# Kernel optimization log

Hardware: AMD Instinct MI355X
Metric: run time of the kernel (lower is better)

Reference implementation:

```python
import jax, jax.numpy as jnp
import numpy as np

TEMPERATURE = 0.1
K = 5  # hard-coded k=5 in ANDCriterion.forward
EPS = 1e-12  # F.normalize eps


def setup_inputs() -> dict:
    key = jax.random.key(0)
    z = jax.random.normal(key, (8192, 1024), dtype=jnp.float32)
    return {"z": z}


def _normalize(z):
    nrm = jnp.sqrt(jnp.sum(z * z, axis=1, keepdims=True))
    return z / jnp.maximum(nrm, EPS)


def reference(z):
    n = z.shape[0]
    zn = _normalize(z)                      # [N, d], L2-normalized rows
    sim = zn @ zn.T                         # [N, N] cosine similarity
    # kNN neighbors (exclude self, which is always the top-1 hit)
    _, idx = jax.lax.top_k(sim, K + 1)      # [N, K+1]
    neigh = idx[:, 1:]                      # [N, K]
    # AND loss: softmax over non-self entries at temperature T;
    # loss_i = -log sum_{j in N(i)} p_ij
    logits = sim / TEMPERATURE
    logits = jnp.where(jnp.eye(n, dtype=bool), -jnp.inf, logits)
    logp = jax.nn.log_softmax(logits, axis=1)           # [N, N]
    neigh_logp = jnp.take_along_axis(logp, neigh, axis=1)  # [N, K]
    loss = -jnp.mean(jax.nn.logsumexp(neigh_logp, axis=1))
    return loss
```

## Files before the change

### kernel.cpp

```cpp
#include <hip/hip_runtime.h>
#include <stdint.h>

#define N_ROWS 8192
#define D_DIM  1024
#define NEG_BIG -1e30f
#define NCHUNK 32
#define CHUNK_J 256
#define NTILE 8
#define BUFSZ 17408

typedef __attribute__((ext_vector_type(16))) float f32x16;
typedef __attribute__((ext_vector_type(8)))  int   i32x8;
typedef __attribute__((ext_vector_type(4)))  int   i32x4;
typedef __attribute__((ext_vector_type(2)))  long  long2_t;

#define EXPC 14.4269504089f
#define EXPRAW(dst, v) { float _a = fmaf((v), EXPC, -EXPC);                 \
    asm("v_exp_f32 %0, %1" : "=v"(dst) : "v"(_a)); }

#define INS5(b0,b1,b2,b3,b4,v) {                        \
    float _n4 = __builtin_amdgcn_fmed3f(b3, (v), b4);   \
    float _n3 = __builtin_amdgcn_fmed3f(b2, (v), b3);   \
    float _n2 = __builtin_amdgcn_fmed3f(b1, (v), b2);   \
    float _n1 = __builtin_amdgcn_fmed3f(b0, (v), b1);   \
    b0 = fmaxf(b0, (v)); b1 = _n1; b2 = _n2; b3 = _n3; b4 = _n4; }

static __device__ inline uint32_t enc4(float x, float inv) {
    float q = fabsf(x) * inv;
    uint32_t n = q < 0.25f ? 0u : (q < 0.75f ? 1u : (q < 1.25f ? 2u : (q < 1.75f ? 3u :
                 (q < 2.5f  ? 4u : (q < 3.5f  ? 5u : (q < 5.0f  ? 6u : 7u))))));
    return n | (x < 0.f ? 8u : 0u);
}

__global__ __launch_bounds__(256) void norm_kernel(const float* __restrict__ z,
                                                   uint8_t* __restrict__ zn4,
                                                   uint8_t* __restrict__ sbq) {
    int wave = threadIdx.x >> 6;
    int lane = threadIdx.x & 63;
    int row  = blockIdx.x * 4 + wave;
    const float* zr = z + (size_t)row * D_DIM;
    float4 c[4];
    float ss = 0.f;
#pragma unroll
    for (int i = 0; i < 4; ++i) {
        c[i] = *(const float4*)(zr + i * 256 + lane * 4);
        ss += c[i].x*c[i].x + c[i].y*c[i].y + c[i].z*c[i].z + c[i].w*c[i].w;
    }
#pragma unroll
    for (int m = 1; m < 64; m <<= 1) ss += __shfl_xor(ss, m);
    float scale = 1.0f / fmaxf(sqrtf(ss), 1e-12f);
    const int J = row >> 5, r31 = row & 31;
    uint8_t* db = zn4 + (size_t)J * 16384;
    uint8_t* sb = sbq + (size_t)J * 1024;
#pragma unroll
    for (int i = 0; i < 4; ++i) {
        float x0 = c[i].x*scale, x1 = c[i].y*scale, x2 = c[i].z*scale, x3 = c[i].w*scale;
        float am = fmaxf(fmaxf(fabsf(x0), fabsf(x1)), fmaxf(fabsf(x2), fabsf(x3)));
        am = fmaxf(am, __shfl_xor(am, 1));
        am = fmaxf(am, __shfl_xor(am, 2));
        am = fmaxf(am, __shfl_xor(am, 4));
        uint32_t ub = __float_as_uint(am);
        int sbyte = (int)(ub >> 23) - 2 + (((ub & 0x7fffffu) > 0x400000u) ? 1 : 0);
        float inv = __uint_as_float((uint32_t)(254 - sbyte) << 23);
        uint32_t pk = enc4(x0, inv) | (enc4(x1, inv) << 4)
                    | (enc4(x2, inv) << 8) | (enc4(x3, inv) << 12);
        int m  = i * 4 + (lane >> 4);
        int l2 = r31 + 32 * ((lane >> 3) & 1);
        *(uint16_t*)(db + m * 1024 + l2 * 16 + 2 * (lane & 7)) = (uint16_t)pk;
        if ((lane & 7) == 0) {
            int j = lane >> 3;
            sb[(size_t)(r31 + 32 * (j & 1)) * 16 + i * 4 + (j >> 1)] = (uint8_t)sbyte;
        }
    }
}

__global__ __launch_bounds__(256, 3) void sim_kernel(const uint8_t* __restrict__ zn4,
                                                     const uint8_t* __restrict__ sbq,
                                                     float* __restrict__ pstats) {
    __shared__ __align__(16) char lds[2 * BUFSZ];
    const int tid  = threadIdx.x;
    const int w    = tid >> 6;
    const int l    = tid & 63;
    const int r32  = l & 31;
    const int h    = l >> 5;
    const int ib   = blockIdx.x >> 5;
    const int ch   = blockIdx.x & 31;
    const int i0w  = ib * 128 + w * 32;
    const int j0c  = ch * CHUNK_J;
    const int i_lane = i0w + r32;
    const int Ii   = ib * 4 + w;
    const int diag_jt = ((Ii >> 3) == ch) ? (Ii & 7) : -1;
    const char* ldsr = lds + l * 16;

#define GLL(SRC, DST) __builtin_amdgcn_global_load_lds(                         \
        (const __attribute__((address_space(1))) uint32_t*)(SRC),               \
        (__attribute__((address_space(3))) uint32_t*)(DST), 16, 0, 0)

#define STAGE(JTN, BUF) {                                                       \
        const uint8_t* sD_ = zn4 + (size_t)(ch * NTILE + (JTN)) * 16384;        \
        _Pragma("unroll")                                                       \
        for (int mm = 0; mm < 4; ++mm) {                                        \
            int m_ = w * 4 + mm;                                                \
            GLL(sD_ + m_ * 1024 + l * 16, (BUF) + m_ * 1024);                   \
        }                                                                       \
        if (w == 0)                                                             \
            GLL(sbq + (size_t)(ch * NTILE + (JTN)) * 1024 + l * 16,             \
                (BUF) + 16384);                                                 \
    }

    STAGE(0, lds);

    i32x8 bres8[8];
    {
        const uint8_t* rp = zn4 + (size_t)Ii * 16384 + l * 16;
#pragma unroll
        for (int g = 0; g < 8; ++g) {
            *(long2_t*)&bres8[g]       = *(const long2_t*)(rp + (2 * g) * 1024);
            *((long2_t*)&bres8[g] + 1) = *(const long2_t*)(rp + (2 * g + 1) * 1024);
        }
    }
    uint32_t sb_[4];
    {
        const uint32_t* sp = (const uint32_t*)(sbq + (size_t)Ii * 1024 + l * 16);
        sb_[0] = sp[0]; sb_[1] = sp[1]; sb_[2] = sp[2]; sb_[3] = sp[3];
    }

    float s0r = 0.f, s1r = 0.f;
    float b0 = NEG_BIG, b1 = NEG_BIG, b2 = NEG_BIG, b3 = NEG_BIG, b4 = NEG_BIG;
    i32x8 areg0 = {0,0,0,0,0,0,0,0}, areg1 = {0,0,0,0,0,0,0,0};
    i32x8 btmp  = {0,0,0,0,0,0,0,0};

    __syncthreads();

#define MFMA_E(M) {                                                             \
        asm volatile("" : "+v"(bres8[(M) >> 1]));                               \
        *(long2_t*)&areg0 = *(const long2_t*)(ldst_ + (M) * 1024);              \
        acc0 = __builtin_amdgcn_mfma_scale_f32_32x32x64_f8f6f4(                 \
            areg0, bres8[(M) >> 1], acc0, 4, 4,                                 \
            (M) & 3, sa_[(M) >> 2], (M) & 3, sb_[(M) >> 2]); }
#define MFMA_O(M) {                                                             \
        *(long2_t*)&btmp  = *((const long2_t*)&bres8[(M) >> 1] + 1);            \
        *(long2_t*)&areg1 = *(const long2_t*)(ldst_ + (M) * 1024);              \
        acc1 = __builtin_amdgcn_mfma_scale_f32_32x32x64_f8f6f4(                 \
            areg1, btmp, acc1, 4, 4,                                            \
            (M) & 3, sa_[(M) >> 2], (M) & 3, sb_[(M) >> 2]); }

#define TILE_BODY(JT, CUR) {                                                    \
        if ((JT) + 1 < NTILE) STAGE((JT) + 1, lds + ((CUR) ^ BUFSZ));           \
        const char* ldst_ = ldsr + (CUR);                                       \
        uint32_t sa_[4];                                                        \
        {                                                                       \
            i32x4 sv = *(const i32x4*)(lds + (CUR) + 16384 + l * 16);           \
            sa_[0] = sv[0]; sa_[1] = sv[1]; sa_[2] = sv[2]; sa_[3] = sv[3];     \
        }                                                                       \
        f32x16 acc0, acc1;                                                      \
        _Pragma("unroll")                                                       \
        for (int r = 0; r < 16; ++r) { acc0[r] = 0.f; acc1[r] = 0.f; }          \
        __builtin_amdgcn_s_setprio(1);                                          \
        MFMA_E(0)  MFMA_O(1)  MFMA_E(2)  MFMA_O(3)                              \
        MFMA_E(4)  MFMA_O(5)  MFMA_E(6)  MFMA_O(7)                              \
        MFMA_E(8)  MFMA_O(9)  MFMA_E(10) MFMA_O(11)                             \
        MFMA_E(12) MFMA_O(13) MFMA_E(14) MFMA_O(15)                             \
        __builtin_amdgcn_s_setprio(0);                                          \
        if ((JT) != diag_jt) {                                                  \
            _Pragma("unroll")                                                   \
            for (int r = 0; r < 16; ++r) {                                      \
                float v = acc0[r] + acc1[r];                                    \
                INS5(b0, b1, b2, b3, b4, v);                                    \
                float e_; EXPRAW(e_, v);                                        \
                if (r & 1) s1r += e_; else s0r += e_;                           \
            }                                                                   \
        } else {                                                                \
            const int dd2 = i_lane - (j0c + (JT) * 32) - 4 * h;                 \
            _Pragma("unroll")                                                   \
            for (int r = 0; r < 16; ++r) {                                      \
                const int jm = (r & 3) + 8 * (r >> 2);                          \
                float v = acc0[r] + acc1[r];                                    \
                if (dd2 == jm) v = NEG_BIG;                                     \
                INS5(b0, b1, b2, b3, b4, v);                                    \
                float e_; EXPRAW(e_, v);                                        \
                if (r & 1) s1r += e_; else s0r += e_;                           \
            }                                                                   \
        }                                                                       \
        __syncthreads();                                                        \
    }

    for (int jt = 0; jt < NTILE; jt += 2) {
        TILE_BODY(jt, 0);
        TILE_BODY(jt + 1, BUFSZ);
    }
#undef TILE_BODY
#undef MFMA_E
#undef MFMA_O
#undef STAGE
#undef GLL

    float s_run = s0r + s1r;
    s_run += __shfl_xor(s_run, 32);
    {
        float o0 = __shfl_xor(b0, 32), o1 = __shfl_xor(b1, 32), o2 = __shfl_xor(b2, 32),
              o3 = __shfl_xor(b3, 32), o4 = __shfl_xor(b4, 32);
        INS5(b0, b1, b2, b3, b4, o0); INS5(b0, b1, b2, b3, b4, o1);
        INS5(b0, b1, b2, b3, b4, o2); INS5(b0, b1, b2, b3, b4, o3);
        INS5(b0, b1, b2, b3, b4, o4);
    }
    if (h == 0) {
        float* p = pstats + ((size_t)ch * N_ROWS + i_lane) * 8;
        p[0] = s_run; p[1] = b0; p[2] = b1; p[3] = b2; p[4] = b3; p[5] = b4;
        p[6] = 0.f; p[7] = 0.f;
    }
}

__global__ __launch_bounds__(128) void reduce1(const float* __restrict__ pstats,
                                               float* __restrict__ partial) {
    int row = blockIdx.x * 128 + threadIdx.x;
    float S = 0.f;
    float b0 = NEG_BIG, b1 = NEG_BIG, b2 = NEG_BIG, b3 = NEG_BIG, b4 = NEG_BIG;
#pragma unroll
    for (int c = 0; c < NCHUNK; ++c) {
        const float* p = pstats + ((size_t)c * N_ROWS + row) * 8;
        S += p[0];
        float v0 = p[1], v1 = p[2], v2 = p[3], v3 = p[4], v4 = p[5];
        INS5(b0, b1, b2, b3, b4, v0); INS5(b0, b1, b2, b3, b4, v1);
        INS5(b0, b1, b2, b3, b4, v2); INS5(b0, b1, b2, b3, b4, v3);
        INS5(b0, b1, b2, b3, b4, v4);
    }
    float e0, e1, e2, e3, e4;
    EXPRAW(e0, b0); EXPRAW(e1, b1); EXPRAW(e2, b2); EXPRAW(e3, b3); EXPRAW(e4, b4);
    float S5 = e0 + e1 + e2 + e3 + e4;
    float loss = __logf(S) - __logf(S5);
#pragma unroll
    for (int m = 1; m < 64; m <<= 1) loss += __shfl_xor(loss, m);
    __shared__ float rr[2];
    if ((threadIdx.x & 63) == 0) rr[threadIdx.x >> 6] = loss;
    __syncthreads();
    if (threadIdx.x == 0) partial[blockIdx.x] = rr[0] + rr[1];
}

__global__ void reduce2(const float* __restrict__ partial, float* __restrict__ out) {
    float v = partial[threadIdx.x];
#pragma unroll
    for (int m = 1; m < 64; m <<= 1) v += __shfl_xor(v, m);
    if (threadIdx.x == 0) out[0] = v * (1.0f / N_ROWS);
}

extern "C" void kernel_launch(void* const* d_in, const int* in_sizes, int n_in,
                              void* d_out, int out_size, void* d_ws, size_t ws_size,
                              hipStream_t stream) {
    const float* z = (const float*)d_in[0];
    float* out = (float*)d_out;
    uint8_t* zn4   = (uint8_t*)d_ws;
    uint8_t* sbq   = (uint8_t*)d_ws + (size_t)4 * 1024 * 1024;
    float* pstats  = (float*)((char*)d_ws + (size_t)4608 * 1024);
    float* partial = (float*)((char*)d_ws + (size_t)13 * 1024 * 1024);

    norm_kernel<<<N_ROWS / 4, 256, 0, stream>>>(z, zn4, sbq);
    sim_kernel<<<64 * NCHUNK, 256, 0, stream>>>(zn4, sbq, pstats);
    reduce1<<<N_ROWS / 128, 128, 0, stream>>>(pstats, partial);
    reduce2<<<1, 64, 0, stream>>>(partial, out);
}
```

Baseline: 69.86 us.

## Fuse final reduction into reduce1 via atomic counter; raise sim occupancy bound

Removes the separate reduce2 launch: each reduce1 block publishes its partial sum with a release store and bumps an atomic counter, and the last block to arrive sums all 64 partials and writes the mean. The counter is reset inside norm_kernel, so it is zero before reduce1 runs. Separately, sim_kernel's launch bounds go from 3 to 4 blocks per SIMD/CU, which pressures the compiler to use fewer registers. That allows more concurrent waves but risks register spills.

Result: slower. 79.69 us (+14.1%).

```diff
diff --git a/kernel.cpp b/kernel.cpp
--- a/kernel.cpp
+++ b/kernel.cpp
@@ -34,7 +34,9 @@
 
 __global__ __launch_bounds__(256) void norm_kernel(const float* __restrict__ z,
                                                    uint8_t* __restrict__ zn4,
-                                                   uint8_t* __restrict__ sbq) {
+                                                   uint8_t* __restrict__ sbq,
+                                                   unsigned* __restrict__ counter) {
+    if (blockIdx.x == 0 && threadIdx.x == 0) *counter = 0;
     int wave = threadIdx.x >> 6;
     int lane = threadIdx.x & 63;
     int row  = blockIdx.x * 4 + wave;
@@ -74,7 +76,7 @@
     }
 }
 
-__global__ __launch_bounds__(256, 3) void sim_kernel(const uint8_t* __restrict__ zn4,
+__global__ __launch_bounds__(256, 4) void sim_kernel(const uint8_t* __restrict__ zn4,
                                                      const uint8_t* __restrict__ sbq,
                                                      float* __restrict__ pstats) {
     __shared__ __align__(16) char lds[2 * BUFSZ];
@@ -85,9 +87,8 @@
     const int h    = l >> 5;
     const int ib   = blockIdx.x >> 5;
     const int ch   = blockIdx.x & 31;
-    const int i0w  = ib * 128 + w * 32;
     const int j0c  = ch * CHUNK_J;
-    const int i_lane = i0w + r32;
+    const int i_lane = ib * 128 + w * 32 + r32;
     const int Ii   = ib * 4 + w;
     const int diag_jt = ((Ii >> 3) == ch) ? (Ii & 7) : -1;
     const char* ldsr = lds + l * 16;
@@ -212,7 +213,9 @@
 }
 
 __global__ __launch_bounds__(128) void reduce1(const float* __restrict__ pstats,
-                                               float* __restrict__ partial) {
+                                               float* __restrict__ partial,
+                                               unsigned* __restrict__ counter,
+                                               float* __restrict__ out) {
     int row = blockIdx.x * 128 + threadIdx.x;
     float S = 0.f;
     float b0 = NEG_BIG, b1 = NEG_BIG, b2 = NEG_BIG, b3 = NEG_BIG, b4 = NEG_BIG;
@@ -234,14 +237,20 @@
     __shared__ float rr[2];
     if ((threadIdx.x & 63) == 0) rr[threadIdx.x >> 6] = loss;
     __syncthreads();
-    if (threadIdx.x == 0) partial[blockIdx.x] = rr[0] + rr[1];
-}
-
-__global__ void reduce2(const float* __restrict__ partial, float* __restrict__ out) {
-    float v = partial[threadIdx.x];
-#pragma unroll
-    for (int m = 1; m < 64; m <<= 1) v += __shfl_xor(v, m);
-    if (threadIdx.x == 0) out[0] = v * (1.0f / N_ROWS);
+    if (threadIdx.x == 0) {
+        float mine = rr[0] + rr[1];
+        __hip_atomic_store(&partial[blockIdx.x], mine,
+                           __ATOMIC_RELEASE, __HIP_MEMORY_SCOPE_AGENT);
+        unsigned prev = __hip_atomic_fetch_add(counter, 1u,
+                           __ATOMIC_ACQ_REL, __HIP_MEMORY_SCOPE_AGENT);
+        if (prev == 63u) {
+            float s = 0.f;
+            for (int i = 0; i < 64; ++i)
+                s += __hip_atomic_load(&partial[i],
+                         __ATOMIC_ACQUIRE, __HIP_MEMORY_SCOPE_AGENT);
+            out[0] = s * (1.0f / N_ROWS);
+        }
+    }
 }
 
 extern "C" void kernel_launch(void* const* d_in, const int* in_sizes, int n_in,
@@ -253,9 +262,9 @@
     uint8_t* sbq   = (uint8_t*)d_ws + (size_t)4 * 1024 * 1024;
     float* pstats  = (float*)((char*)d_ws + (size_t)4608 * 1024);
     float* partial = (float*)((char*)d_ws + (size_t)13 * 1024 * 1024);
-
-    norm_kernel<<<N_ROWS / 4, 256, 0, stream>>>(z, zn4, sbq);
+    unsigned* counter = (unsigned*)((char*)d_ws + (size_t)13 * 1024 * 1024 + 256);
+
+    norm_kernel<<<N_ROWS / 4, 256, 0, stream>>>(z, zn4, sbq, counter);
     sim_kernel<<<64 * NCHUNK, 256, 0, stream>>>(zn4, sbq, pstats);
-    reduce1<<<N_ROWS / 128, 128, 0, stream>>>(pstats, partial);
-    reduce2<<<1, 64, 0, stream>>>(partial, out);
-}
+    reduce1<<<N_ROWS / 128, 128, 0, stream>>>(pstats, partial, counter, out);
+}
```

## Widen column chunks, prefetch A operands ahead, skip top-5 insert when unneeded

Applied to the files above, without the earlier changes.

Doubles the column chunk per block from 256 to 512 (16 tiles), which halves the grid and the partial-stat entries, and lowers launch bounds to 2 waves per SIMD. The MFMA loop now keeps four A registers and loads each operand four MFMAs ahead from LDS, so LDS latency overlaps with matrix work. The top-5 insertion is skipped for a tile unless some lane's tile max beats its current fifth-best value, which avoids many med3 ops. The costs are more register pressure and lower occupancy, and the 50 unseen lines (the reduction kernel) must agree with the new NCHUNK.

After: 69.57 us. About the same (-0.4%).

```diff
diff --git a/kernel.cpp b/kernel.cpp
--- a/kernel.cpp
+++ b/kernel.cpp
@@ -4,9 +4,9 @@
 #define N_ROWS 8192
 #define D_DIM  1024
 #define NEG_BIG -1e30f
-#define NCHUNK 32
-#define CHUNK_J 256
-#define NTILE 8
+#define NCHUNK 16
+#define CHUNK_J 512
+#define NTILE 16
 #define BUFSZ 17408
 
 typedef __attribute__((ext_vector_type(16))) float f32x16;
@@ -74,7 +74,7 @@
     }
 }
 
-__global__ __launch_bounds__(256, 3) void sim_kernel(const uint8_t* __restrict__ zn4,
+__global__ __launch_bounds__(256, 2) void sim_kernel(const uint8_t* __restrict__ zn4,
                                                      const uint8_t* __restrict__ sbq,
                                                      float* __restrict__ pstats) {
     __shared__ __align__(16) char lds[2 * BUFSZ];
@@ -83,13 +83,12 @@
     const int l    = tid & 63;
     const int r32  = l & 31;
     const int h    = l >> 5;
-    const int ib   = blockIdx.x >> 5;
-    const int ch   = blockIdx.x & 31;
-    const int i0w  = ib * 128 + w * 32;
+    const int ib   = blockIdx.x >> 4;
+    const int ch   = blockIdx.x & 15;
     const int j0c  = ch * CHUNK_J;
-    const int i_lane = i0w + r32;
+    const int i_lane = ib * 128 + w * 32 + r32;
     const int Ii   = ib * 4 + w;
-    const int diag_jt = ((Ii >> 3) == ch) ? (Ii & 7) : -1;
+    const int diag_jt = ((Ii >> 4) == ch) ? (Ii & 15) : -1;
     const char* ldsr = lds + l * 16;
 
 #define GLL(SRC, DST) __builtin_amdgcn_global_load_lds(                         \
@@ -127,23 +126,24 @@
 
     float s0r = 0.f, s1r = 0.f;
     float b0 = NEG_BIG, b1 = NEG_BIG, b2 = NEG_BIG, b3 = NEG_BIG, b4 = NEG_BIG;
-    i32x8 areg0 = {0,0,0,0,0,0,0,0}, areg1 = {0,0,0,0,0,0,0,0};
-    i32x8 btmp  = {0,0,0,0,0,0,0,0};
+    i32x8 a0 = {0,0,0,0,0,0,0,0}, a1 = {0,0,0,0,0,0,0,0};
+    i32x8 a2 = {0,0,0,0,0,0,0,0}, a3 = {0,0,0,0,0,0,0,0};
+    i32x8 btmp = {0,0,0,0,0,0,0,0};
 
     __syncthreads();
 
-#define MFMA_E(M) {                                                             \
+#define MFMA_EV(M, AR, RF) {                                                    \
         asm volatile("" : "+v"(bres8[(M) >> 1]));                               \
-        *(long2_t*)&areg0 = *(const long2_t*)(ldst_ + (M) * 1024);              \
         acc0 = __builtin_amdgcn_mfma_scale_f32_32x32x64_f8f6f4(                 \
-            areg0, bres8[(M) >> 1], acc0, 4, 4,                                 \
-            (M) & 3, sa_[(M) >> 2], (M) & 3, sb_[(M) >> 2]); }
-#define MFMA_O(M) {                                                             \
-        *(long2_t*)&btmp  = *((const long2_t*)&bres8[(M) >> 1] + 1);            \
-        *(long2_t*)&areg1 = *(const long2_t*)(ldst_ + (M) * 1024);              \
+            AR, bres8[(M) >> 1], acc0, 4, 4,                                    \
+            (M) & 3, sa_[(M) >> 2], (M) & 3, sb_[(M) >> 2]);                    \
+        if ((RF) >= 0) *(long2_t*)&AR = *(const long2_t*)(ldst_ + (RF) * 1024); }
+#define MFMA_OD(M, AR, RF) {                                                    \
+        *(long2_t*)&btmp = *((const long2_t*)&bres8[(M) >> 1] + 1);             \
         acc1 = __builtin_amdgcn_mfma_scale_f32_32x32x64_f8f6f4(                 \
-            areg1, btmp, acc1, 4, 4,                                            \
-            (M) & 3, sa_[(M) >> 2], (M) & 3, sb_[(M) >> 2]); }
+            AR, btmp, acc1, 4, 4,                                               \
+            (M) & 3, sa_[(M) >> 2], (M) & 3, sb_[(M) >> 2]);                    \
+        if ((RF) >= 0) *(long2_t*)&AR = *(const long2_t*)(ldst_ + (RF) * 1024); }
 
 #define TILE_BODY(JT, CUR) {                                                    \
         if ((JT) + 1 < NTILE) STAGE((JT) + 1, lds + ((CUR) ^ BUFSZ));           \
@@ -153,34 +153,46 @@
             i32x4 sv = *(const i32x4*)(lds + (CUR) + 16384 + l * 16);           \
             sa_[0] = sv[0]; sa_[1] = sv[1]; sa_[2] = sv[2]; sa_[3] = sv[3];     \
         }                                                                       \
+                                   \
+        *(long2_t*)&a0 = *(const long2_t*)(ldst_ + 0 * 1024);                   \
+        *(long2_t*)&a1 = *(const long2_t*)(ldst_ + 1 * 1024);                   \
+        *(long2_t*)&a2 = *(const long2_t*)(ldst_ + 2 * 1024);                   \
+        *(long2_t*)&a3 = *(const long2_t*)(ldst_ + 3 * 1024);                   \
         f32x16 acc0, acc1;                                                      \
         _Pragma("unroll")                                                       \
         for (int r = 0; r < 16; ++r) { acc0[r] = 0.f; acc1[r] = 0.f; }          \
         __builtin_amdgcn_s_setprio(1);                                          \
-        MFMA_E(0)  MFMA_O(1)  MFMA_E(2)  MFMA_O(3)                              \
-        MFMA_E(4)  MFMA_O(5)  MFMA_E(6)  MFMA_O(7)                              \
-        MFMA_E(8)  MFMA_O(9)  MFMA_E(10) MFMA_O(11)                             \
-        MFMA_E(12) MFMA_O(13) MFMA_E(14) MFMA_O(15)                             \
+        MFMA_EV(0,  a0, 4)   MFMA_OD(1,  a1, 5)                                 \
+        MFMA_EV(2,  a2, 6)   MFMA_OD(3,  a3, 7)                                 \
+        MFMA_EV(4,  a0, 8)   MFMA_OD(5,  a1, 9)                                 \
+        MFMA_EV(6,  a2, 10)  MFMA_OD(7,  a3, 11)                                \
+        MFMA_EV(8,  a0, 12)  MFMA_OD(9,  a1, 13)                                \
+        MFMA_EV(10, a2, 14)  MFMA_OD(11, a3, 15)                                \
+        MFMA_EV(12, a0, -1)  MFMA_OD(13, a1, -1)                                \
+        MFMA_EV(14, a2, -1)  MFMA_OD(15, a3, -1)                                \
         __builtin_amdgcn_s_setprio(0);                                          \
-        if ((JT) != diag_jt) {                                                  \
-            _Pragma("unroll")                                                   \
-            for (int r = 0; r < 16; ++r) {                                      \
-                float v = acc0[r] + acc1[r];                                    \
-                INS5(b0, b1, b2, b3, b4, v);                                    \
-                float e_; EXPRAW(e_, v);                                        \
-                if (r & 1) s1r += e_; else s0r += e_;                           \
-            }                                                                   \
-        } else {                                                                \
+        f32x16 vv;                                                              \
+        _Pragma("unroll")                                                       \
+        for (int r = 0; r < 16; ++r) vv[r] = acc0[r] + acc1[r];                 \
+        if ((JT) == diag_jt) {                                                  \
             const int dd2 = i_lane - (j0c + (JT) * 32) - 4 * h;                 \
             _Pragma("unroll")                                                   \
             for (int r = 0; r < 16; ++r) {                                      \
                 const int jm = (r & 3) + 8 * (r >> 2);                          \
-                float v = acc0[r] + acc1[r];                                    \
-                if (dd2 == jm) v = NEG_BIG;                                     \
-                INS5(b0, b1, b2, b3, b4, v);                                    \
-                float e_; EXPRAW(e_, v);                                        \
-                if (r & 1) s1r += e_; else s0r += e_;                           \
+                if (dd2 == jm) vv[r] = NEG_BIG;                                 \
             }                                                                   \
+        }                                                                       \
+        float mx_ = vv[0];                                                      \
+        _Pragma("unroll")                                                       \
+        for (int r = 1; r < 16; ++r) mx_ = fmaxf(mx_, vv[r]);                   \
+        if (__any(mx_ > b4)) {                          \
+            _Pragma("unroll")                                                   \
+            for (int r = 0; r < 16; ++r) { INS5(b0, b1, b2, b3, b4, vv[r]); }   \
+        }                                                                       \
+        _Pragma("unroll")                                                       \
+        for (int r = 0; r < 16; ++r) {                                          \
+            float e_; EXPRAW(e_, vv[r]);                                        \
+            if (r & 1) s1r += e_; else s0r += e_;                               \
         }                                                                       \
         __syncthreads();                                                        \
     }
@@ -190,8 +202,8 @@
         TILE_BODY(jt + 1, BUFSZ);
     }
 #undef TILE_BODY
-#undef MFMA_E
-#undef MFMA_O
+#undef MFMA_EV
+#undef MFMA_OD
 #undef STAGE
 #undef GLL
 
```
